# Performance work log

Hardware: AMD Instinct MI355X
Metric: run time of the kernel (lower is better)

## Reference

```python
import jax, jax.numpy as jnp
import numpy as np

def setup_inputs() -> dict:
    key = jax.random.key(0)
    ks = jax.random.split(key, 8)
    B, C, H, W = 4, 64, 64, 64
    Cr = C // 8
    s = 1.0 / np.sqrt(C)
    return {
        "x": jax.random.normal(ks[0], (B, C, H, W), jnp.float32),
        "wq": jax.random.normal(ks[1], (Cr, C), jnp.float32) * s,
        "bq": jax.random.normal(ks[2], (Cr,), jnp.float32) * 0.01,
        "wk": jax.random.normal(ks[3], (Cr, C), jnp.float32) * s,
        "bk": jax.random.normal(ks[4], (Cr,), jnp.float32) * 0.01,
        "wv": jax.random.normal(ks[5], (C, C), jnp.float32) * s,
        "bv": jax.random.normal(ks[6], (C,), jnp.float32) * 0.01,
        "gamma": jax.random.normal(ks[7], (1,), jnp.float32) * 0.1,
    }

def reference(x, wq, bq, wk, bk, wv, bv, gamma):
    B, C, H, W = x.shape
    N = H * W
    xf = x.reshape(B, C, N)  # 1x1 conv == pointwise linear over channel dim
    q = jnp.einsum("oc,bcn->bno", wq, xf) + bq[None, None, :]   # (B, N, Cr)
    k = jnp.einsum("oc,bcn->bon", wk, xf) + bk[None, :, None]   # (B, Cr, N)
    v = jnp.einsum("oc,bcn->bon", wv, xf) + bv[None, :, None]   # (B, C, N)
    attn = jnp.einsum("bno,bom->bnm", q, k)                     # (B, N, N)
    attn = jax.nn.softmax(attn, axis=-1)
    out = jnp.einsum("bcm,bnm->bcn", v, attn)                   # (B, C, N)
    out = out.reshape(B, C, H, W)
    return x + gamma[0] * out
```

## Files before the change

### kernel.cpp

```cpp
#include <hip/hip_runtime.h>

#define BB 4
#define CC 64
#define NN 4096

typedef __attribute__((ext_vector_type(8)))  short short8;
typedef __attribute__((ext_vector_type(4)))  short short4v;
typedef __attribute__((ext_vector_type(4)))  float f32x4;
typedef __attribute__((ext_vector_type(16))) float f32x16;
typedef unsigned short u16;

#define QWS_ELEMS (BB * NN * 8)

__device__ inline u16 f2bf(float x) {
    unsigned u = __float_as_uint(x);
    u = (u + 0x7fffu + ((u >> 16) & 1u)) >> 16;
    return (u16)u;
}
__device__ inline unsigned pack2rne(float a, float b) {
    return (unsigned)f2bf(a) | ((unsigned)f2bf(b) << 16);
}
__device__ inline unsigned permpack(float lo, float hi) {
    return __builtin_amdgcn_perm(__float_as_uint(hi), __float_as_uint(lo), 0x07060302);
}

__device__ inline void barrier_lgkm() {
    asm volatile("s_waitcnt lgkmcnt(0)\n\ts_barrier" ::: "memory");
}

union SH8 {
    short8 s;
    struct Halves { short4v lo, hi; } h;
    uint4 u;
};

__global__ __launch_bounds__(512) void proj_kernel(
    const float* __restrict__ x,
    const float* __restrict__ wq, const float* __restrict__ bq,
    const float* __restrict__ wk, const float* __restrict__ bk,
    const float* __restrict__ wv, const float* __restrict__ bv,
    u16* __restrict__ ws_u)
{
    u16* qws = ws_u;
    u16* kws = ws_u + QWS_ELEMS;
    u16* vws = ws_u + 2 * QWS_ELEMS;

    const int y   = blockIdx.y;
    const int pix = blockIdx.x * 512 + threadIdx.x;
    const int b   = pix >> 12;
    const int n   = pix & (NN - 1);
    const float* xb = x + ((size_t)b << 18) + n;

    const int v0  = y << 3;
    const int isq = (y < 4) ? 1 : 0;
    const int qc0 = (y & 3) << 1;
    const float* wj = isq ? wq : wk;
    const float* bj = isq ? bq : bk;

    float av[8];
    float a0 = bj[qc0], a1 = bj[qc0 + 1];
#pragma unroll
    for (int i = 0; i < 8; ++i) av[i] = bv[v0 + i];
#pragma unroll 8
    for (int c = 0; c < CC; ++c) {
        const float xv = xb[(size_t)c << 12];
#pragma unroll
        for (int i = 0; i < 8; ++i)
            av[i] += wv[(v0 + i) * CC + c] * xv;
        a0 += wj[qc0 * CC + c] * xv;
        a1 += wj[(qc0 + 1) * CC + c] * xv;
    }
#pragma unroll
    for (int i = 0; i < 8; ++i)
        vws[(((size_t)((b << 6) + v0 + i)) << 12) + n] = f2bf(av[i]);

    u16* dst = (isq ? qws : kws) + (size_t)pix * 8 + qc0;
    *(unsigned*)dst = pack2rne(a0, a1);
}

__global__ __launch_bounds__(512) void attn_kernel(
    const float* __restrict__ x, const float* __restrict__ gamma,
    const u16* __restrict__ ws_u, float* __restrict__ out)
{
    const u16* qws = ws_u;
    const u16* kws = ws_u + QWS_ELEMS;
    const u16* vws = ws_u + 2 * QWS_ELEMS;

    __shared__ __align__(16) char smem[34816 + 1024 + 256];
    u16*   v_t    = (u16*)smem;
    float* eb     = (float*)smem;
    float* eb2    = (float*)smem;
    float* l_part = (float*)(smem + 34816);
    float* l_inv  = (float*)(smem + 34816 + 1024);

    const int tid  = threadIdx.x;
    const int w    = tid >> 6;
    const int lane = tid & 63;
    const int l31  = lane & 31;
    const int lh   = lane >> 5;
    const int mh   = w >> 1;
    const int qh   = w & 1;

    const int b  = blockIdx.y;
    const int qb = blockIdx.x << 6;
    const int bN = b << 12;

    short8 qf = {0,0,0,0,0,0,0,0};
    short8 kf = {0,0,0,0,0,0,0,0};
    if (lane < 32) {
        qf = *(const short8*)(qws + (size_t)(bN + qb + (qh << 5) + l31) * 8);
        kf = *(const short8*)(kws + (size_t)(bN + (mh << 5) + l31) * 8);
    }
    short8 kn = kf;

    const int c_st = tid >> 3;
    const int o_st = (tid & 7) << 3;
    const u16* vgr = vws + (((size_t)((b << 6) + c_st)) << 12) + o_st;
    const int st0  = c_st * 132 + o_st;

    SH8 va0, va1, vb0, vb1;
    va0.s = *(const short8*)(vgr);
    va1.s = *(const short8*)(vgr + 64);
    *(short4v*)&v_t[st0]      = va0.h.lo;
    *(short4v*)&v_t[st0 + 4]  = va0.h.hi;
    *(short4v*)&v_t[st0 + 64] = va1.h.lo;
    *(short4v*)&v_t[st0 + 68] = va1.h.hi;
    va0.s = *(const short8*)(vgr + 128);
    va1.s = *(const short8*)(vgr + 192);

    const int rA = l31 * 132;
    const int rB = (32 + l31) * 132;
    const int mb = (mh << 5) + (lh << 2);

    f32x16 z16, acc0, acc1;
#pragma unroll
    for (int r = 0; r < 16; ++r) { z16[r] = 0.f; acc0[r] = 0.f; acc1[r] = 0.f; }
    float ls = 0.f;

    barrier_lgkm();

#pragma unroll 2
    for (int it = 0; it < 32; ++it) {
        const int buf = (it & 1) * (CC * 132);
        const int nxt = ((it + 1) & 31) << 7;
        const int nx2 = ((it + 2) & 31) << 7;

        vb0.s = *(const short8*)(vgr + nx2);
        vb1.s = *(const short8*)(vgr + nx2 + 64);
        if (lane < 32)
            kn = *(const short8*)(kws + (size_t)(bN + nxt + (mh << 5) + l31) * 8);

        f32x16 d = __builtin_amdgcn_mfma_f32_32x32x16_bf16(kf, qf, z16, 0, 0, 0);

        float p[16];
#pragma unroll
        for (int r = 0; r < 16; ++r) p[r] = __expf(d[r]);
        float s0 = 0.f, s1 = 0.f;
#pragma unroll
        for (int r = 0; r < 8; ++r) { s0 += p[2 * r]; s1 += p[2 * r + 1]; }
        ls += s0 + s1;

        SH8 A0, A1;
        A0.u.x = permpack(p[0],  p[1]);  A0.u.y = permpack(p[2],  p[3]);
        A0.u.z = permpack(p[4],  p[5]);  A0.u.w = permpack(p[6],  p[7]);
        A1.u.x = permpack(p[8],  p[9]);  A1.u.y = permpack(p[10], p[11]);
        A1.u.z = permpack(p[12], p[13]); A1.u.w = permpack(p[14], p[15]);

        SH8 B00, B01, B10, B11;
        B00.h.lo = *(const short4v*)&v_t[buf + rA + mb];
        B00.h.hi = *(const short4v*)&v_t[buf + rA + mb + 8];
        B01.h.lo = *(const short4v*)&v_t[buf + rB + mb];
        B01.h.hi = *(const short4v*)&v_t[buf + rB + mb + 8];
        B10.h.lo = *(const short4v*)&v_t[buf + rA + mb + 16];
        B10.h.hi = *(const short4v*)&v_t[buf + rA + mb + 24];
        B11.h.lo = *(const short4v*)&v_t[buf + rB + mb + 16];
        B11.h.hi = *(const short4v*)&v_t[buf + rB + mb + 24];

        acc0 = __builtin_amdgcn_mfma_f32_32x32x16_bf16(A0.s, B00.s, acc0, 0, 0, 0);
        acc1 = __builtin_amdgcn_mfma_f32_32x32x16_bf16(A0.s, B01.s, acc1, 0, 0, 0);
        acc0 = __builtin_amdgcn_mfma_f32_32x32x16_bf16(A1.s, B10.s, acc0, 0, 0, 0);
        acc1 = __builtin_amdgcn_mfma_f32_32x32x16_bf16(A1.s, B11.s, acc1, 0, 0, 0);

        const int ob = (CC * 132) - buf;
        *(short4v*)&v_t[ob + st0]      = va0.h.lo;
        *(short4v*)&v_t[ob + st0 + 4]  = va0.h.hi;
        *(short4v*)&v_t[ob + st0 + 64] = va1.h.lo;
        *(short4v*)&v_t[ob + st0 + 68] = va1.h.hi;
        va0 = vb0; va1 = vb1;
        kf = kn;

        barrier_lgkm();
    }

    float lt = ls + __shfl_xor(ls, 32, 64);
    if (lane < 32) l_part[(mh * 2 + qh) * 32 + l31] = lt;
    __syncthreads();
    if (w < 2 && lane < 32) {
        float s = l_part[(0 * 2 + qh) * 32 + l31] + l_part[(1 * 2 + qh) * 32 + l31]
                + l_part[(2 * 2 + qh) * 32 + l31] + l_part[(3 * 2 + qh) * 32 + l31];
        l_inv[qh * 32 + l31] = gamma[0] / s;
    }

    if (mh >= 2) {
        float* e0 = &eb[(((mh - 2) << 2) + (qh << 1) + 0) * 1088 + lane * 17];
        float* e1 = &eb[(((mh - 2) << 2) + (qh << 1) + 1) * 1088 + lane * 17];
#pragma unroll
        for (int r = 0; r < 16; ++r) { e0[r] = acc0[r]; e1[r] = acc1[r]; }
    }
    __syncthreads();
    if (mh < 2) {
        const float* e0 = &eb[((mh << 2) + (qh << 1) + 0) * 1088 + lane * 17];
        const float* e1 = &eb[((mh << 2) + (qh << 1) + 1) * 1088 + lane * 17];
#pragma unroll
        for (int r = 0; r < 16; ++r) { acc0[r] += e0[r]; acc1[r] += e1[r]; }
    }
    __syncthreads();
    if (mh == 1) {
        float* e0 = &eb[((qh << 1) + 0) * 1088 + lane * 17];
        float* e1 = &eb[((qh << 1) + 1) * 1088 + lane * 17];
#pragma unroll
        for (int r = 0; r < 16; ++r) { e0[r] = acc0[r]; e1[r] = acc1[r]; }
    }
    __syncthreads();
    if (w < 2) {
        const float* e0 = &eb[((qh << 1) + 0) * 1088 + lane * 17];
        const float* e1 = &eb[((qh << 1) + 1) * 1088 + lane * 17];
#pragma unroll
        for (int r = 0; r < 16; ++r) { acc0[r] += e0[r]; acc1[r] += e1[r]; }
    }
    __syncthreads();

    if (w < 2) {
        f32x4 li[4];
#pragma unroll
        for (int k = 0; k < 4; ++k)
            li[k] = *(const f32x4*)&l_inv[qh * 32 + (k << 3) + (lh << 2)];
#pragma unroll
        for (int ch = 0; ch < 2; ++ch) {
            const int c = (ch << 5) + l31;
            const f32x16 a = ch ? acc1 : acc0;
            float* er = eb2 + c * 69 + (qh << 5) + (lh << 2);
#pragma unroll
            for (int k = 0; k < 4; ++k) {
#pragma unroll
                for (int r = 0; r < 4; ++r)
                    er[(k << 3) + r] = a[4 * k + r] * li[k][r];
            }
        }
    }
    __syncthreads();

    {
        const int c2 = tid >> 3;
        const int qo = (tid & 7) << 3;
        const float* er = eb2 + c2 * 69 + qo;
        const size_t rowb = (((size_t)((b << 6) + c2)) << 12) + qb + qo;
        const float4 x0 = *(const float4*)&x[rowb];
        const float4 x1 = *(const float4*)&x[rowb + 4];
        float4 o0, o1;
        o0.x = x0.x + er[0]; o0.y = x0.y + er[1];
        o0.z = x0.z + er[2]; o0.w = x0.w + er[3];
        o1.x = x1.x + er[4]; o1.y = x1.y + er[5];
        o1.z = x1.z + er[6]; o1.w = x1.w + er[7];
        *(float4*)&out[rowb]     = o0;
        *(float4*)&out[rowb + 4] = o1;
    }
}

extern "C" void kernel_launch(void* const* d_in, const int* in_sizes, int n_in,
                              void* d_out, int out_size, void* d_ws, size_t ws_size,
                              hipStream_t stream)
{
    const float* x     = (const float*)d_in[0];
    const float* wq    = (const float*)d_in[1];
    const float* bq    = (const float*)d_in[2];
    const float* wk    = (const float*)d_in[3];
    const float* bk    = (const float*)d_in[4];
    const float* wv    = (const float*)d_in[5];
    const float* bv    = (const float*)d_in[6];
    const float* gamma = (const float*)d_in[7];
    u16*   ws  = (u16*)d_ws;
    float* out = (float*)d_out;

    hipLaunchKernelGGL(proj_kernel, dim3(BB * NN / 512, 8), dim3(512), 0, stream,
                       x, wq, bq, wk, bk, wv, bv, ws);
    hipLaunchKernelGGL(attn_kernel, dim3(NN / 64, BB), dim3(512), 0, stream,
                       x, gamma, ws, out);
}
```

Measured before the change: 99.89 us.

## Process two key tiles per barrier and fold log2e into Q for exp2

The attention loop now handles two 128-key subtiles per iteration. LDS staging of V doubles to four buffers, so there are half as many block-wide barriers. Q is pre-scaled by log2(e) in the projection kernel so the softmax can use a native exp2 instead of __expf. Row sums use a packed two-wide float accumulator. The cost is doubled shared memory (about 68KB per block), which may reduce occupancy, plus more registers for the extra prefetched V and K fragments.

```diff
diff --git a/kernel.cpp b/kernel.cpp
--- a/kernel.cpp
+++ b/kernel.cpp
@@ -6,11 +6,19 @@
 
 typedef __attribute__((ext_vector_type(8)))  short short8;
 typedef __attribute__((ext_vector_type(4)))  short short4v;
+typedef __attribute__((ext_vector_type(2)))  float f32x2;
 typedef __attribute__((ext_vector_type(4)))  float f32x4;
 typedef __attribute__((ext_vector_type(16))) float f32x16;
 typedef unsigned short u16;
 
 #define QWS_ELEMS (BB * NN * 8)
+#define LOG2E 1.4426950408889634f
+
+#if __has_builtin(__builtin_amdgcn_exp2f)
+#define EXP2(x) __builtin_amdgcn_exp2f(x)
+#else
+#define EXP2(x) __expf((x) * 0.6931471805599453f)
+#endif
 
 __device__ inline u16 f2bf(float x) {
     unsigned u = __float_as_uint(x);
@@ -74,9 +82,12 @@
     for (int i = 0; i < 8; ++i)
         vws[(((size_t)((b << 6) + v0 + i)) << 12) + n] = f2bf(av[i]);
 
+    if (isq) { a0 *= LOG2E; a1 *= LOG2E; }
     u16* dst = (isq ? qws : kws) + (size_t)pix * 8 + qc0;
     *(unsigned*)dst = pack2rne(a0, a1);
 }
+
+#define CC132 (CC * 132)
 
 __global__ __launch_bounds__(512) void attn_kernel(
     const float* __restrict__ x, const float* __restrict__ gamma,
@@ -86,12 +97,12 @@
     const u16* kws = ws_u + QWS_ELEMS;
     const u16* vws = ws_u + 2 * QWS_ELEMS;
 
-    __shared__ __align__(16) char smem[34816 + 1024 + 256];
+    __shared__ __align__(16) char smem[67584 + 1024 + 256];
     u16*   v_t    = (u16*)smem;
     float* eb     = (float*)smem;
     float* eb2    = (float*)smem;
-    float* l_part = (float*)(smem + 34816);
-    float* l_inv  = (float*)(smem + 34816 + 1024);
+    float* l_part = (float*)(smem + 67584);
+    float* l_inv  = (float*)(smem + 67584 + 1024);
 
     const int tid  = threadIdx.x;
     const int w    = tid >> 6;
@@ -105,28 +116,38 @@
     const int qb = blockIdx.x << 6;
     const int bN = b << 12;
 
-    short8 qf = {0,0,0,0,0,0,0,0};
-    short8 kf = {0,0,0,0,0,0,0,0};
+    short8 qf  = {0,0,0,0,0,0,0,0};
+    short8 kf0 = {0,0,0,0,0,0,0,0};
+    short8 kf1 = {0,0,0,0,0,0,0,0};
     if (lane < 32) {
-        qf = *(const short8*)(qws + (size_t)(bN + qb + (qh << 5) + l31) * 8);
-        kf = *(const short8*)(kws + (size_t)(bN + (mh << 5) + l31) * 8);
-    }
-    short8 kn = kf;
+        qf  = *(const short8*)(qws + (size_t)(bN + qb + (qh << 5) + l31) * 8);
+        kf0 = *(const short8*)(kws + (size_t)(bN + (mh << 5) + l31) * 8);
+        kf1 = *(const short8*)(kws + (size_t)(bN + 128 + (mh << 5) + l31) * 8);
+    }
+    short8 kn0 = kf0, kn1 = kf1;
 
     const int c_st = tid >> 3;
     const int o_st = (tid & 7) << 3;
     const u16* vgr = vws + (((size_t)((b << 6) + c_st)) << 12) + o_st;
     const int st0  = c_st * 132 + o_st;
 
-    SH8 va0, va1, vb0, vb1;
+    SH8 va0, va1, va2, va3, vb0, vb1, vb2, vb3;
     va0.s = *(const short8*)(vgr);
     va1.s = *(const short8*)(vgr + 64);
-    *(short4v*)&v_t[st0]      = va0.h.lo;
-    *(short4v*)&v_t[st0 + 4]  = va0.h.hi;
-    *(short4v*)&v_t[st0 + 64] = va1.h.lo;
-    *(short4v*)&v_t[st0 + 68] = va1.h.hi;
-    va0.s = *(const short8*)(vgr + 128);
-    va1.s = *(const short8*)(vgr + 192);
+    va2.s = *(const short8*)(vgr + 128);
+    va3.s = *(const short8*)(vgr + 192);
+    *(short4v*)&v_t[st0]              = va0.h.lo;
+    *(short4v*)&v_t[st0 + 4]          = va0.h.hi;
+    *(short4v*)&v_t[st0 + 64]         = va1.h.lo;
+    *(short4v*)&v_t[st0 + 68]         = va1.h.hi;
+    *(short4v*)&v_t[CC132 + st0]      = va2.h.lo;
+    *(short4v*)&v_t[CC132 + st0 + 4]  = va2.h.hi;
+    *(short4v*)&v_t[CC132 + st0 + 64] = va3.h.lo;
+    *(short4v*)&v_t[CC132 + st0 + 68] = va3.h.hi;
+    va0.s = *(const short8*)(vgr + 256);
+    va1.s = *(const short8*)(vgr + 320);
+    va2.s = *(const short8*)(vgr + 384);
+    va3.s = *(const short8*)(vgr + 448);
 
     const int rA = l31 * 132;
     const int rB = (32 + l31) * 132;
@@ -135,62 +156,78 @@
     f32x16 z16, acc0, acc1;
 #pragma unroll
     for (int r = 0; r < 16; ++r) { z16[r] = 0.f; acc0[r] = 0.f; acc1[r] = 0.f; }
-    float ls = 0.f;
+    f32x2 ls2 = {0.f, 0.f};
 
     barrier_lgkm();
 
+#define SUBTILE(KF, BUFOFF)                                                    \
+    {                                                                          \
+        f32x16 d = __builtin_amdgcn_mfma_f32_32x32x16_bf16(KF, qf, z16, 0, 0, 0); \
+        float p[16];                                                           \
+        _Pragma("unroll")                                                      \
+        for (int r = 0; r < 16; ++r) p[r] = EXP2(d[r]);                        \
+        f32x2 s2 = {0.f, 0.f};                                                 \
+        _Pragma("unroll")                                                      \
+        for (int r = 0; r < 8; ++r) {                                          \
+            f32x2 t = {p[2 * r], p[2 * r + 1]};                                \
+            s2 += t;                                                           \
+        }                                                                      \
+        ls2 += s2;                                                             \
+        SH8 A0, A1;                                                            \
+        A0.u.x = permpack(p[0],  p[1]);  A0.u.y = permpack(p[2],  p[3]);       \
+        A0.u.z = permpack(p[4],  p[5]);  A0.u.w = permpack(p[6],  p[7]);       \
+        A1.u.x = permpack(p[8],  p[9]);  A1.u.y = permpack(p[10], p[11]);      \
+        A1.u.z = permpack(p[12], p[13]); A1.u.w = permpack(p[14], p[15]);      \
+        SH8 B00, B01, B10, B11;                                                \
+        B00.h.lo = *(const short4v*)&v_t[(BUFOFF) + rA + mb];                  \
+        B00.h.hi = *(const short4v*)&v_t[(BUFOFF) + rA + mb + 8];              \
+        B01.h.lo = *(const short4v*)&v_t[(BUFOFF) + rB + mb];                  \
+        B01.h.hi = *(const short4v*)&v_t[(BUFOFF) + rB + mb + 8];              \
+        B10.h.lo = *(const short4v*)&v_t[(BUFOFF) + rA + mb + 16];             \
+        B10.h.hi = *(const short4v*)&v_t[(BUFOFF) + rA + mb + 24];             \
+        B11.h.lo = *(const short4v*)&v_t[(BUFOFF) + rB + mb + 16];             \
+        B11.h.hi = *(const short4v*)&v_t[(BUFOFF) + rB + mb + 24];             \
+        acc0 = __builtin_amdgcn_mfma_f32_32x32x16_bf16(A0.s, B00.s, acc0, 0, 0, 0); \
+        acc1 = __builtin_amdgcn_mfma_f32_32x32x16_bf16(A0.s, B01.s, acc1, 0, 0, 0); \
+        acc0 = __builtin_amdgcn_mfma_f32_32x32x16_bf16(A1.s, B10.s, acc0, 0, 0, 0); \
+        acc1 = __builtin_amdgcn_mfma_f32_32x32x16_bf16(A1.s, B11.s, acc1, 0, 0, 0); \
+    }
+
 #pragma unroll 2
-    for (int it = 0; it < 32; ++it) {
-        const int buf = (it & 1) * (CC * 132);
-        const int nxt = ((it + 1) & 31) << 7;
-        const int nx2 = ((it + 2) & 31) << 7;
-
-        vb0.s = *(const short8*)(vgr + nx2);
-        vb1.s = *(const short8*)(vgr + nx2 + 64);
-        if (lane < 32)
-            kn = *(const short8*)(kws + (size_t)(bN + nxt + (mh << 5) + l31) * 8);
-
-        f32x16 d = __builtin_amdgcn_mfma_f32_32x32x16_bf16(kf, qf, z16, 0, 0, 0);
-
-        float p[16];
-#pragma unroll
-        for (int r = 0; r < 16; ++r) p[r] = __expf(d[r]);
-        float s0 = 0.f, s1 = 0.f;
-#pragma unroll
-        for (int r = 0; r < 8; ++r) { s0 += p[2 * r]; s1 += p[2 * r + 1]; }
-        ls += s0 + s1;
-
-        SH8 A0, A1;
-        A0.u.x = permpack(p[0],  p[1]);  A0.u.y = permpack(p[2],  p[3]);
-        A0.u.z = permpack(p[4],  p[5]);  A0.u.w = permpack(p[6],  p[7]);
-        A1.u.x = permpack(p[8],  p[9]);  A1.u.y = permpack(p[10], p[11]);
-        A1.u.z = permpack(p[12], p[13]); A1.u.w = permpack(p[14], p[15]);
-
-        SH8 B00, B01, B10, B11;
-        B00.h.lo = *(const short4v*)&v_t[buf + rA + mb];
-        B00.h.hi = *(const short4v*)&v_t[buf + rA + mb + 8];
-        B01.h.lo = *(const short4v*)&v_t[buf + rB + mb];
-        B01.h.hi = *(const short4v*)&v_t[buf + rB + mb + 8];
-        B10.h.lo = *(const short4v*)&v_t[buf + rA + mb + 16];
-        B10.h.hi = *(const short4v*)&v_t[buf + rA + mb + 24];
-        B11.h.lo = *(const short4v*)&v_t[buf + rB + mb + 16];
-        B11.h.hi = *(const short4v*)&v_t[buf + rB + mb + 24];
-
-        acc0 = __builtin_amdgcn_mfma_f32_32x32x16_bf16(A0.s, B00.s, acc0, 0, 0, 0);
-        acc1 = __builtin_amdgcn_mfma_f32_32x32x16_bf16(A0.s, B01.s, acc1, 0, 0, 0);
-        acc0 = __builtin_amdgcn_mfma_f32_32x32x16_bf16(A1.s, B10.s, acc0, 0, 0, 0);
-        acc1 = __builtin_amdgcn_mfma_f32_32x32x16_bf16(A1.s, B11.s, acc1, 0, 0, 0);
-
-        const int ob = (CC * 132) - buf;
-        *(short4v*)&v_t[ob + st0]      = va0.h.lo;
-        *(short4v*)&v_t[ob + st0 + 4]  = va0.h.hi;
-        *(short4v*)&v_t[ob + st0 + 64] = va1.h.lo;
-        *(short4v*)&v_t[ob + st0 + 68] = va1.h.hi;
-        va0 = vb0; va1 = vb1;
-        kf = kn;
+    for (int i = 0; i < 16; ++i) {
+        const int pb = (i & 1) * (2 * CC132);
+        const int ob = (2 * CC132) - pb;
+        const int nk = ((2 * i + 2) & 31) << 7;
+        const int nv = ((2 * i + 4) & 31) << 7;
+
+        vb0.s = *(const short8*)(vgr + nv);
+        vb1.s = *(const short8*)(vgr + nv + 64);
+        vb2.s = *(const short8*)(vgr + nv + 128);
+        vb3.s = *(const short8*)(vgr + nv + 192);
+        if (lane < 32) {
+            kn0 = *(const short8*)(kws + (size_t)(bN + nk + (mh << 5) + l31) * 8);
+            kn1 = *(const short8*)(kws + (size_t)(bN + nk + 128 + (mh << 5) + l31) * 8);
+        }
+
+        SUBTILE(kf0, pb)
+        SUBTILE(kf1, pb + CC132)
+
+        *(short4v*)&v_t[ob + st0]              = va0.h.lo;
+        *(short4v*)&v_t[ob + st0 + 4]          = va0.h.hi;
+        *(short4v*)&v_t[ob + st0 + 64]         = va1.h.lo;
+        *(short4v*)&v_t[ob + st0 + 68]         = va1.h.hi;
+        *(short4v*)&v_t[ob + CC132 + st0]      = va2.h.lo;
+        *(short4v*)&v_t[ob + CC132 + st0 + 4]  = va2.h.hi;
+        *(short4v*)&v_t[ob + CC132 + st0 + 64] = va3.h.lo;
+        *(short4v*)&v_t[ob + CC132 + st0 + 68] = va3.h.hi;
+        va0 = vb0; va1 = vb1; va2 = vb2; va3 = vb3;
+        kf0 = kn0; kf1 = kn1;
 
         barrier_lgkm();
     }
+#undef SUBTILE
+
+    float ls = ls2.x + ls2.y;
 
     float lt = ls + __shfl_xor(ls, 32, 64);
     if (lane < 32) l_part[(mh * 2 + qh) * 32 + l31] = lt;
```

After: 96.00 us. 3.9% less time.
